# Kernel optimization log

Hardware: AMD Instinct MI355X
Metric: run time of the kernel (lower is better)

## Reference

```python
import jax, jax.numpy as jnp
import numpy as np

N, E, D, EDGE_DIM = 50000, 150000, 100, 200

def _w(key, fi, fo):
    return jax.random.normal(key, (fi, fo), dtype=jnp.float32) / np.float32(np.sqrt(fi))

def setup_inputs():
    key = jax.random.key(0)
    ks = jax.random.split(key, 40)
    inp = {}
    inp["x"] = jax.random.normal(ks[0], (N, D), dtype=jnp.float32)
    inp["msg"] = jax.random.normal(ks[1], (E, D), dtype=jnp.float32)
    # TimeEncoder: Linear(1, D)
    inp["time_w"] = _w(ks[2], 1, D)
    inp["time_b"] = jnp.zeros((D,), jnp.float32)
    # TransformerConv 1: in=100, heads=8, out=100, concat -> 800
    H1 = 8 * D
    inp["c1_qw"] = _w(ks[3], D, H1); inp["c1_qb"] = jnp.zeros((H1,), jnp.float32)
    inp["c1_kw"] = _w(ks[4], D, H1); inp["c1_kb"] = jnp.zeros((H1,), jnp.float32)
    inp["c1_vw"] = _w(ks[5], D, H1); inp["c1_vb"] = jnp.zeros((H1,), jnp.float32)
    inp["c1_ew"] = _w(ks[6], EDGE_DIM, H1)  # lin_edge has no bias in PyG
    inp["c1_sw"] = _w(ks[7], D, H1); inp["c1_sb"] = jnp.zeros((H1,), jnp.float32)
    # TransformerConv 2: in=800, heads=1, out=100, concat=False
    inp["c2_qw"] = _w(ks[8], H1, D); inp["c2_qb"] = jnp.zeros((D,), jnp.float32)
    inp["c2_kw"] = _w(ks[9], H1, D); inp["c2_kb"] = jnp.zeros((D,), jnp.float32)
    inp["c2_vw"] = _w(ks[10], H1, D); inp["c2_vb"] = jnp.zeros((D,), jnp.float32)
    inp["c2_ew"] = _w(ks[11], EDGE_DIM, D)
    inp["c2_sw"] = _w(ks[12], H1, D); inp["c2_sb"] = jnp.zeros((D,), jnp.float32)
    # LinkPredictor (in_channels=100, out=2)
    inp["lp_src_w"] = _w(ks[13], D, 2 * D); inp["lp_src_b"] = jnp.zeros((2 * D,), jnp.float32)
    inp["lp_dst_w"] = _w(ks[14], D, 2 * D); inp["lp_dst_b"] = jnp.zeros((2 * D,), jnp.float32)
    inp["lp1_w"] = _w(ks[15], 4 * D, 8 * D); inp["lp1_b"] = jnp.zeros((8 * D,), jnp.float32)
    inp["lp2_w"] = _w(ks[16], 8 * D, 2 * D); inp["lp2_b"] = jnp.zeros((2 * D,), jnp.float32)
    inp["lp3_w"] = _w(ks[17], 2 * D, D // 2); inp["lp3_b"] = jnp.zeros((D // 2,), jnp.float32)
    inp["lp4_w"] = _w(ks[18], D // 2, 2); inp["lp4_b"] = jnp.zeros((2,), jnp.float32)
    inp["last_update"] = jax.random.randint(ks[19], (N,), 0, 1000000)
    inp["t"] = jax.random.randint(ks[20], (E,), 0, 1000000)
    inp["edge_index"] = jax.random.randint(ks[21], (2, E), 0, N)
    return inp

def _tconv(x, src, dst, edge_attr, qw, qb, kw, kb, vw, vb, ew, sw, sb, heads, out_ch, concat, n):
    q = (x @ qw + qb).reshape(n, heads, out_ch)
    k = (x @ kw + kb).reshape(n, heads, out_ch)
    v = (x @ vw + vb).reshape(n, heads, out_ch)
    e = (edge_attr @ ew).reshape(-1, heads, out_ch)        # [E,H,C]
    kj = k[src] + e                                        # gather src keys + edge
    alpha = jnp.sum(q[dst] * kj, axis=-1) / np.float32(np.sqrt(out_ch))  # [E,H]
    amax = jax.ops.segment_max(alpha, dst, num_segments=n)
    ex = jnp.exp(alpha - amax[dst])
    denom = jax.ops.segment_sum(ex, dst, num_segments=n)
    a = ex / (denom[dst] + 1e-16)                          # per-dest softmax
    agg = jax.ops.segment_sum((v[src] + e) * a[..., None], dst, num_segments=n)
    out = agg.reshape(n, heads * out_ch) if concat else jnp.mean(agg, axis=1)
    return out + x @ sw + sb                               # root/skip connection

def reference(x, msg, time_w, time_b,
              c1_qw, c1_qb, c1_kw, c1_kb, c1_vw, c1_vb, c1_ew, c1_sw, c1_sb,
              c2_qw, c2_qb, c2_kw, c2_kb, c2_vw, c2_vb, c2_ew, c2_sw, c2_sb,
              lp_src_w, lp_src_b, lp_dst_w, lp_dst_b,
              lp1_w, lp1_b, lp2_w, lp2_b, lp3_w, lp3_b, lp4_w, lp4_b,
              last_update, t, edge_index):
    src, dst = edge_index[0], edge_index[1]
    rel_t = (last_update[src] - t).astype(jnp.float32)[:, None]  # [E,1]
    rel_enc = jnp.cos(rel_t @ time_w + time_b)                   # [E,D]
    edge_attr = jnp.concatenate([rel_enc, msg], axis=-1)         # [E,200]
    h = jax.nn.relu(_tconv(x, src, dst, edge_attr, c1_qw, c1_qb, c1_kw, c1_kb,
                           c1_vw, c1_vb, c1_ew, c1_sw, c1_sb, 8, D, True, N))
    h = jax.nn.relu(_tconv(h, src, dst, edge_attr, c2_qw, c2_qb, c2_kw, c2_kb,
                           c2_vw, c2_vb, c2_ew, c2_sw, c2_sb, 1, D, False, N))
    hh = jnp.concatenate([h[src] @ lp_src_w + lp_src_b,
                          h[dst] @ lp_dst_w + lp_dst_b], axis=-1)
    hh = jnp.tanh(hh @ lp1_w + lp1_b)
    hh = jnp.tanh(hh @ lp2_w + lp2_b)
    hh = jnp.tanh(hh @ lp3_w + lp3_b)
    return hh @ lp4_w + lp4_b
```

## Files before the change

### kernel.cpp

```cpp
#include <hip/hip_runtime.h>
#include <hip/hip_bf16.h>
#include <math.h>

typedef __hip_bfloat16 bf16;
typedef short s16x8 __attribute__((ext_vector_type(8)));
typedef float f32x4 __attribute__((ext_vector_type(4)));

#define NN 50000
#define EE 150000
#define EH 75000

static __device__ __forceinline__ float b2f(bf16 x){ return __bfloat162float(x); }
static __device__ __forceinline__ bf16 f2b(float x){ return __float2bfloat16(x); }
static __device__ __forceinline__ short f2s(float x){
  union { bf16 b; short s; } u; u.b = f2b(x); return u.s;
}
static __device__ __forceinline__ float u2f_lo(unsigned u){ union{unsigned i;float f;}c; c.i=u<<16; return c.f; }
static __device__ __forceinline__ float u2f_hi(unsigned u){ union{unsigned i;float f;}c; c.i=u&0xffff0000u; return c.f; }

static __device__ __forceinline__ float fast_tanh(float x){
  float a = fabsf(x);
  float e = __expf(2.0f*a);
  float t = 1.0f - __fdividef(2.0f, e + 1.0f);
  return x < 0.f ? -t : t;
}

static __device__ __forceinline__ void gload_lds16(const void* g, void* l){
  __builtin_amdgcn_global_load_lds((const __attribute__((address_space(1))) void*)g,
                                   (__attribute__((address_space(3))) void*)l, 16, 0, 0);
}

template<int N> static __device__ __forceinline__ void wait_vmcnt(){
  if constexpr(N==0) asm volatile("s_waitcnt vmcnt(0)" ::: "memory");
  else if constexpr(N==1) asm volatile("s_waitcnt vmcnt(1)" ::: "memory");
  else if constexpr(N==2) asm volatile("s_waitcnt vmcnt(2)" ::: "memory");
  else if constexpr(N==3) asm volatile("s_waitcnt vmcnt(3)" ::: "memory");
  else if constexpr(N==4) asm volatile("s_waitcnt vmcnt(4)" ::: "memory");
  else if constexpr(N==5) asm volatile("s_waitcnt vmcnt(5)" ::: "memory");
  else asm volatile("s_waitcnt vmcnt(6)" ::: "memory");
}
static __device__ __forceinline__ void wait_lgkm0(){
  asm volatile("s_waitcnt lgkmcnt(0)" ::: "memory");
}
static __device__ __forceinline__ void memfence(){
  asm volatile("" ::: "memory");
}

__global__ void k_zero(int* __restrict__ p, int n){
  int i = blockIdx.x*blockDim.x + threadIdx.x;
  if(i<n) p[i]=0;
}

__global__ void k_hist(const int* __restrict__ dst, int* __restrict__ deg){
  int i = blockIdx.x*blockDim.x + threadIdx.x;
  if(i<EE) atomicAdd(&deg[dst[i]], 1);
}

__global__ void k_scan(const int* __restrict__ deg, int* __restrict__ rowptr){
  __shared__ int part[1024];
  int tid = threadIdx.x;
  const int n = NN;
  int chunk = (n + 1023)/1024;
  int start = tid*chunk;
  int end = start + chunk; if(end > n) end = n;
  int s = 0;
  for(int i=start;i<end;i++) s += deg[i];
  part[tid] = s; __syncthreads();
  for(int off=1; off<1024; off<<=1){
    int v = (tid>=off)? part[tid-off] : 0;
    __syncthreads();
    part[tid] += v;
    __syncthreads();
  }
  int run = (tid==0)? 0 : part[tid-1];
  for(int i=start;i<end;i++){ rowptr[i]=run; run += deg[i]; }
  if(tid==0) rowptr[n] = part[1023];
}

__global__ void k_scatter(const int* __restrict__ dst, const int* __restrict__ rowptr,
                          int* __restrict__ cursor, int* __restrict__ elist){
  int e = blockIdx.x*blockDim.x + threadIdx.x;
  if(e<EE){ int d=dst[e]; int p=atomicAdd(&cursor[d],1); elist[rowptr[d]+p]=e; }
}

__global__ void k_relenc(const int* __restrict__ src, const int* __restrict__ tt,
                         const int* __restrict__ lu, const float* __restrict__ tw,
                         const float* __restrict__ tb, bf16* __restrict__ rel){
  int i = blockIdx.x*blockDim.x + threadIdx.x;
  if(i >= EE*112) return;
  int e = i/112, c = i - e*112;
  float v = 0.f;
  if(c < 100){
    float rt  = (float)(lu[src[e]] - tt[e]);
    float arg = __fadd_rn(__fmul_rn(rt, tw[c]), tb[c]);
    v = cosf(arg);
  }
  rel[i] = f2b(v);
}

__global__ void k_cvtpad(const float* __restrict__ in, int incols,
                         bf16* __restrict__ outp, int outcols, int total){
  int i = blockIdx.x*blockDim.x + threadIdx.x;
  if(i >= total) return;
  int r = i/outcols, c = i - r*outcols;
  outp[i] = f2b(c < incols ? in[(size_t)r*incols + c] : 0.f);
}

__global__ void k_wt2(const float* __restrict__ W, int K, int N, int colofs, int ncols,
                      bf16* __restrict__ WT, int kpad, int nrows){
  int i = blockIdx.x*blockDim.x + threadIdx.x;
  if(i >= nrows*kpad) return;
  int n = i / kpad, k = i - n*kpad;
  float v = (n<ncols && k<K)? W[(size_t)k*N + colofs + n] : 0.f;
  WT[i] = f2b(v);
}

__global__ void k_wtc1(const float* __restrict__ qw, const float* __restrict__ kw,
                       const float* __restrict__ vw, const float* __restrict__ sw,
                       bf16* __restrict__ outp){
  int i = blockIdx.x*blockDim.x + threadIdx.x;
  if(i >= 8*448*128) return;
  int h = i/(448*128), r = (i/128)%448, k = i&127;
  float v = 0.f;
  if(r < 400 && k < 100){
    int s = r/100, n = r - s*100;
    const float* W = s==0? qw : s==1? kw : s==2? vw : sw;
    v = W[(size_t)k*800 + h*100 + n];
  }
  outp[i] = f2b(v);
}

__global__ void k_wte(const float* __restrict__ ew, int N, int colofs,
                      bf16* __restrict__ outp){
  int i = blockIdx.x*blockDim.x + threadIdx.x;
  if(i >= 112*256) return;
  int r = i>>8, k = i&255;
  float v = 0.f;
  if(r < 100){
    if(k < 100) v = ew[(size_t)k*N + colofs + r];
    else if(k >= 128 && k < 228) v = ew[(size_t)(k-28)*N + colofs + r];
  }
  outp[i] = f2b(v);
}

__global__ void k_bstack(const float* __restrict__ b0, const float* __restrict__ b1,
                         const float* __restrict__ b2, const float* __restrict__ b3,
                         int W, int H, float* __restrict__ outp){
  int i = blockIdx.x*blockDim.x + threadIdx.x;
  if(i >= H*4*W) return;
  int h = i/(4*W), r = i - h*4*W, s = r/W, c = r - s*W;
  const float* b = s==0? b0 : s==1? b1 : s==2? b2 : b3;
  outp[i] = b[h*W + c];
}

__global__ void k_foldw(const float* __restrict__ sw, const float* __restrict__ dw,
                        const float* __restrict__ w1, bf16* __restrict__ o){
  int i = blockIdx.x*blockDim.x + threadIdx.x;
  if(i >= 800*224) return;
  int n = i/224, k = i - n*224;
  float s = 0.f;
  if(k < 100){
    for(int j=0;j<200;j++) s += sw[k*200+j]*w1[(size_t)j*800+n];
  } else if(k >= 112 && k < 212){
    int kk = k-112;
    for(int j=0;j<200;j++) s += dw[kk*200+j]*w1[(size_t)(200+j)*800+n];
  }
  o[i] = f2b(s);
}
__global__ void k_foldb(const float* __restrict__ sb, const float* __restrict__ db,
                        const float* __restrict__ w1, const float* __restrict__ b1,
                        float* __restrict__ o){
  int n = blockIdx.x*blockDim.x + threadIdx.x;
  if(n >= 800) return;
  float s = b1[n];
  for(int j=0;j<200;j++) s += sb[j]*w1[(size_t)j*800+n] + db[j]*w1[(size_t)(200+j)*800+n];
  o[n] = s;
}

template<int NT>
__global__ __launch_bounds__(256) void mm_tile(
    const bf16* __restrict__ A1, int lda1, int kv1, const int* __restrict__ g1,
    int KS,
    const bf16* __restrict__ A2b, int lda2b, int kv2b, const int* __restrict__ g2,
    const float* __restrict__ A2f, int lda2f, int kv2f,
    const bf16* __restrict__ WT, int kpad,
    const bf16* __restrict__ zbuf,
    const float* __restrict__ bias,
    bf16* __restrict__ C, int ldc,
    int M, int nvalid, int act)
{
  constexpr int BN = NT*16;
  constexpr int BPASS = (BN*4 + 255)/256;
  constexpr int ABYTES = 8192;
  constexpr int BUFSZ = ABYTES + BPASS*4096;
  __shared__ __align__(16) char lds[3*BUFSZ];

  const int tid  = threadIdx.x;
  const int wave = tid>>6, lane = tid&63;
  const int quad = lane>>4, lo = lane&15;
  const int nstrip = blockIdx.y;
  WT += (size_t)nstrip*BN*kpad;
  C  += (size_t)nstrip*BN;
  if(bias) bias += nstrip*BN;
  const int nval = nvalid - nstrip*BN;
  const int row0 = blockIdx.x*128;

  float bvr[NT];
#pragma unroll
  for(int n=0;n<NT;n++){
    int col = n*16 + lo;
    bvr[n] = (bias && col < nval) ? bias[col] : 0.f;
  }
#pragma unroll
  for(int n=0;n<NT;n++) asm volatile("" :: "v"(bvr[n]));

  const char*  a1b[2];
  const char*  a2b[2];
  const float* f2base[2];
  int acol0[2];
#pragma unroll
  for(int p=0;p<2;p++){
    int s = p*256 + tid;
    int row = s>>2, cp = s&3;
    int q = cp ^ ((row>>1)&3);
    int col0 = q*8;
    int rg = row0 + row; if(rg > M-1) rg = M-1;
    int r1 = g1 ? g1[rg] : rg;
    int r2 = g2 ? g2[rg] : rg;
    acol0[p] = col0;
    a1b[p]   = (const char*)A1 + ((size_t)r1*lda1 + col0)*2;
    a2b[p]   = A2b ? (const char*)A2b + ((size_t)r2*lda2b)*2 : nullptr;
    f2base[p]= A2f ? (A2f + (size_t)rg*lda2f) : nullptr;
  }
  const char* bbase[BPASS];
#pragma unroll
  for(int p=0;p<BPASS;p++){
    int s = p*256 + tid;
    int rb = s>>2; if(rb > BN-1) rb = BN-1;
    int cp = s&3;
    int lq = cp ^ ((rb>>1)&3);
    bbase[p] = (const char*)WT + ((size_t)rb*kpad + lq*8)*2;
  }

  f32x4 acc[2][NT];
#pragma unroll
  for(int m=0;m<2;m++)
#pragma unroll
    for(int n=0;n<NT;n++) acc[m][n] = (f32x4){0.f,0.f,0.f,0.f};

  float4 pf0[2], pf1[2];

  auto stageA1 = [&](char* buf, int kb){
#pragma unroll
    for(int p=0;p<2;p++){
      int k = kb + acol0[p];
      const char* s;
      if(k < KS) s = (k < kv1) ? (a1b[p] + (size_t)kb*2) : (const char*)zbuf;
      else { int o = k - KS; s = (o < kv2b) ? (a2b[p] + (size_t)o*2) : (const char*)zbuf; }
      gload_lds16(s, buf + p*4096 + wave*1024);
    }
  };
  auto loadA2f = [&](int kb){
#pragma unroll
    for(int p=0;p<2;p++){
      int o = kb + acol0[p] - KS;
      const float* ap = f2base[p] + o;
      pf0[p] = (o   < kv2f) ? *(const float4*)ap     : (float4){0.f,0.f,0.f,0.f};
      pf1[p] = (o+4 < kv2f) ? *(const float4*)(ap+4) : (float4){0.f,0.f,0.f,0.f};
    }
  };
  auto writeA2 = [&](char* buf){
#pragma unroll
    for(int p=0;p<2;p++){
      s16x8 v;
      v[0]=f2s(pf0[p].x); v[1]=f2s(pf0[p].y); v[2]=f2s(pf0[p].z); v[3]=f2s(pf0[p].w);
      v[4]=f2s(pf1[p].x); v[5]=f2s(pf1[p].y); v[6]=f2s(pf1[p].z); v[7]=f2s(pf1[p].w);
      *(s16x8*)(buf + p*4096 + (size_t)tid*16) = v;
    }
  };
  auto stageB = [&](char* buf, int kb){
#pragma unroll
    for(int p=0;p<BPASS;p++)
      gload_lds16(bbase[p] + (size_t)kb*2, buf + ABYTES + p*4096 + wave*1024);
  };
  auto compute = [&](const char* buf){
    s16x8 af[2];
#pragma unroll
    for(int m=0;m<2;m++){
      int rl = wave*32 + m*16 + lo;
      int cp = quad ^ ((rl>>1)&3);
      af[m] = *(const s16x8*)(buf + rl*64 + cp*16);
    }
#pragma unroll
    for(int n=0;n<NT;n++){
      int rb = n*16 + lo;
      int cp = quad ^ ((rb>>1)&3);
      s16x8 bfr = *(const s16x8*)(buf + ABYTES + rb*64 + cp*16);
      acc[0][n] = __builtin_amdgcn_mfma_f32_16x16x32_bf16(af[0], bfr, acc[0][n], 0,0,0);
      acc[1][n] = __builtin_amdgcn_mfma_f32_16x16x32_bf16(af[1], bfr, acc[1][n], 0,0,0);
    }
  };

  const int T = kpad >> 5;
  stageA1(lds, 0); stageB(lds, 0);
  if(T > 1){ stageA1(lds + BUFSZ, 32); stageB(lds + BUFSZ, 32); }

  for(int t=0; t<T; t++){
    bool nb  = (t+1 < T);
    bool nfp = nb && A2f && (((t+1)<<5) >= KS);
    if(!nb)      wait_vmcnt<0>();
    else if(nfp) wait_vmcnt<BPASS>();
    else         wait_vmcnt<2+BPASS>();
    wait_lgkm0();
    __builtin_amdgcn_s_barrier();
    memfence();
    int tp = t+2;
    bool sp  = (tp < T);
    bool spf = sp && A2f && ((tp<<5) >= KS);
    char* nb3 = lds + (tp%3)*BUFSZ;
    if(sp){
      int kb2 = tp<<5;
      if(spf) loadA2f(kb2);
      else    stageA1(nb3, kb2);
      stageB(nb3, kb2);
    }
    compute(lds + (t%3)*BUFSZ);
    if(spf) writeA2(nb3);
  }

  const int r0 = (lane&1)<<1;
#pragma unroll
  for(int n=0;n<NT;n++){
    int col  = n*16 + lo;
    int pcol = col & ~1;
    bool cok = (pcol < nval);
    float bv = bvr[n];
#pragma unroll
    for(int m=0;m<2;m++){
      float v[4];
#pragma unroll
      for(int r=0;r<4;r++){
        float t = acc[m][n][r] + bv;
        if(act==1) t = fmaxf(t, 0.f);
        else if(act==2) t = fast_tanh(t);
        v[r] = t;
      }
      unsigned mylo = (unsigned)(unsigned short)f2s(v[r0])
                    | ((unsigned)(unsigned short)f2s(v[r0+1])<<16);
      unsigned snd  = (unsigned)(unsigned short)f2s(v[r0^2])
                    | ((unsigned)(unsigned short)f2s(v[(r0^2)+1])<<16);
      unsigned got  = (unsigned)__shfl_xor((int)snd, 1);
      unsigned w0, w1;
      if(lane&1){ w0 = (got & 0xffffu) | (mylo<<16); w1 = (got>>16) | (mylo & 0xffff0000u); }
      else      { w0 = (mylo & 0xffffu) | (got<<16); w1 = (mylo>>16) | (got & 0xffff0000u); }
      if(cok){
        int prow = row0 + wave*32 + m*16 + quad*4 + r0;
        if(prow   < M) *(unsigned*)(C + (size_t)prow*ldc + pcol) = w0;
        if(prow+1 < M) *(unsigned*)(C + (size_t)(prow+1)*ldc + pcol) = w1;
      }
    }
  }
}

__global__ __launch_bounds__(256) void k_attn(
    const int* __restrict__ rowptr, const int* __restrict__ elist,
    const int* __restrict__ srcv,
    const bf16* __restrict__ qkvs, const bf16* __restrict__ eh,
    bf16* __restrict__ hout, int ldh, int colofs, int zpad)
{
  int wave = threadIdx.x>>6, lane = threadIdx.x&63;
  int node = blockIdx.x*4 + wave;
  if(node >= NN) return;
  bool act = (lane < 50);
  float q0=0.f, q1=0.f;
  const unsigned* qrow = (const unsigned*)(qkvs + (size_t)node*400);
  if(act){ unsigned u = qrow[lane]; q0=u2f_lo(u); q1=u2f_hi(u); }
  int s0 = rowptr[node], s1 = rowptr[node+1];
  float m = -3.4e38f, d = 0.f, a0 = 0.f, a1 = 0.f;
  for(int j=s0; j<s1; j++){
    int e = elist[j];
    int sn = srcv[e];
    float p = 0.f, e0=0.f, e1=0.f;
    if(act){
      unsigned uk = ((const unsigned*)(qkvs + (size_t)sn*400 + 100))[lane];
      unsigned ue = ((const unsigned*)(eh   + (size_t)e*100))[lane];
      e0=u2f_lo(ue); e1=u2f_hi(ue);
      p = q0*(u2f_lo(uk)+e0) + q1*(u2f_hi(uk)+e1);
    }
    for(int off=32; off; off>>=1) p += __shfl_xor(p, off);
    float alpha = p * 0.1f;
    float mn = fmaxf(m, alpha);
    float sc = __expf(m - mn);
    float wv = __expf(alpha - mn);
    d = d*sc + wv;
    if(act){
      unsigned uv = ((const unsigned*)(qkvs + (size_t)sn*400 + 200))[lane];
      a0 = a0*sc + wv*(u2f_lo(uv)+e0);
      a1 = a1*sc + wv*(u2f_hi(uv)+e1);
    }
    m = mn;
  }
  if(act){
    float inv = 1.f/(d + 1e-16f);
    unsigned us = ((const unsigned*)(qkvs + (size_t)node*400 + 300))[lane];
    float h0 = fmaxf(u2f_lo(us) + a0*inv, 0.f);
    float h1 = fmaxf(u2f_hi(us) + a1*inv, 0.f);
    bf16* op = hout + (size_t)node*ldh + colofs + lane*2;
    op[0] = f2b(h0); op[1] = f2b(h1);
  } else if(zpad && lane < 56){
    bf16* op = hout + (size_t)node*ldh + colofs + lane*2;
    op[0] = f2b(0.f); op[1] = f2b(0.f);
  }
}

__global__ void k_lpout(const bf16* __restrict__ t3, const float* __restrict__ w4,
                        const float* __restrict__ b4, float* __restrict__ out,
                        int base, int n){
  int i = blockIdx.x*blockDim.x + threadIdx.x;
  if(i >= n*2) return;
  int g = i>>1, j = i&1;
  const bf16* tp = t3 + (size_t)g*50;
  float s = 0.f;
  for(int k=0;k<50;k++) s += b2f(tp[k])*w4[k*2+j];
  out[(size_t)(base+g)*2 + j] = s + b4[j];
}

extern "C" void kernel_launch(void* const* d_in, const int* in_sizes, int n_in,
                              void* d_out, int out_size, void* d_ws, size_t ws_size,
                              hipStream_t stream){
  const float* x       = (const float*)d_in[0];
  const float* msg     = (const float*)d_in[1];
  const float* time_w  = (const float*)d_in[2];
  const float* time_b  = (const float*)d_in[3];
  const float* c1_qw=(const float*)d_in[4];  const float* c1_qb=(const float*)d_in[5];
  const float* c1_kw=(const float*)d_in[6];  const float* c1_kb=(const float*)d_in[7];
  const float* c1_vw=(const float*)d_in[8];  const float* c1_vb=(const float*)d_in[9];
  const float* c1_ew=(const float*)d_in[10];
  const float* c1_sw=(const float*)d_in[11]; const float* c1_sb=(const float*)d_in[12];
  const float* c2_qw=(const float*)d_in[13]; const float* c2_qb=(const float*)d_in[14];
  const float* c2_kw=(const float*)d_in[15]; const float* c2_kb=(const float*)d_in[16];
  const float* c2_vw=(const float*)d_in[17]; const float* c2_vb=(const float*)d_in[18];
  const float* c2_ew=(const float*)d_in[19];
  const float* c2_sw=(const float*)d_in[20]; const float* c2_sb=(const float*)d_in[21];
  const float* lp_src_w=(const float*)d_in[22]; const float* lp_src_b=(const float*)d_in[23];
  const float* lp_dst_w=(const float*)d_in[24]; const float* lp_dst_b=(const float*)d_in[25];
  const float* lp1_w=(const float*)d_in[26]; const float* lp1_b=(const float*)d_in[27];
  const float* lp2_w=(const float*)d_in[28]; const float* lp2_b=(const float*)d_in[29];
  const float* lp3_w=(const float*)d_in[30]; const float* lp3_b=(const float*)d_in[31];
  const float* lp4_w=(const float*)d_in[32]; const float* lp4_b=(const float*)d_in[33];
  const int* last_update=(const int*)d_in[34];
  const int* tt =(const int*)d_in[35];
  const int* edge_index=(const int*)d_in[36];
  const int* src = edge_index;
  const int* dst = edge_index + EE;
  float* out = (float*)d_out;

  char* ws = (char*)d_ws;
  bf16*  h1    = (bf16*) (ws + 0);
  bf16*  relpad= (bf16*) (ws + 80000000);
  bf16*  eh    = (bf16*) (ws + 113600000);
  bf16*  qkvs  = (bf16*) (ws + 143600000);
  bf16*  h2p   = (bf16*) (ws + 183600000);
  bf16*  xb    = (bf16*) (ws + 183600000);
  int*   rowptr= (int*)  (ws + 194800000);
  int*   elist = (int*)  (ws + 195000064);
  int*   deg   = (int*)  (ws + 195600064);
  int*   cursor= (int*)  (ws + 195800064);
  bf16* c1all  = (bf16*)(ws + 196000064);
  bf16* c1eall = (bf16*)(ws + 196917568);
  bf16* c2all  = (bf16*)(ws + 197376320);
  bf16* c2e    = (bf16*)(ws + 198179136);
  bf16* lp1tF  = (bf16*)(ws + 198351168);
  bf16* lp2t   = (bf16*)(ws + 199268672);
  bf16* lp3t   = (bf16*)(ws + 199670080);
  float* c1ball= (float*)(ws + 199702848);
  float* c2ball= (float*)(ws + 199715648);
  bf16* zbuf   = (bf16*)(ws + 199717248);
  float* lp1c  = (float*)(ws + 199717312);
  bf16* lt1 = (bf16*)(ws + 0);
  bf16* lt2 = (bf16*)(ws + 120000000);
  bf16* lt3 = (bf16*)(ws + 150000000);

  k_wtc1<<<(8*448*128+255)/256,256,0,stream>>>(c1_qw,c1_kw,c1_vw,c1_sw,c1all);
  for(int h=0; h<8; h++)
    k_wte<<<(112*256+255)/256,256,0,stream>>>(c1_ew, 800, h*100, c1eall + (size_t)h*112*256);
  k_wte<<<(112*256+255)/256,256,0,stream>>>(c2_ew, 100, 0, c2e);
  k_wt2<<<(100*800+255)/256,256,0,stream>>>(c2_qw,800,100,0,100,c2all,         800,100);
  k_wt2<<<(100*800+255)/256,256,0,stream>>>(c2_kw,800,100,0,100,c2all+100*800, 800,100);
  k_wt2<<<(100*800+255)/256,256,0,stream>>>(c2_vw,800,100,0,100,c2all+200*800, 800,100);
  k_wt2<<<(100*800+255)/256,256,0,stream>>>(c2_sw,800,100,0,100,c2all+300*800, 800,100);
  k_wt2<<<(48*800+255)/256,256,0,stream>>>(c2_sw,800,100,0,0,   c2all+400*800, 800,48);
  k_wt2<<<(224*800+255)/256,256,0,stream>>>(lp2_w,800,200,0,200,lp2t,800,224);
  k_wt2<<<(64*224+255)/256,256,0,stream>>>(lp3_w,200,50,0,50,lp3t,224,64);
  k_foldw<<<(800*224+255)/256,256,0,stream>>>(lp_src_w, lp_dst_w, lp1_w, lp1tF);
  k_foldb<<<(800+255)/256,256,0,stream>>>(lp_src_b, lp_dst_b, lp1_w, lp1_b, lp1c);
  k_bstack<<<(3200+255)/256,256,0,stream>>>(c1_qb,c1_kb,c1_vb,c1_sb,100,8,c1ball);
  k_bstack<<<(400+255)/256,256,0,stream>>>(c2_qb,c2_kb,c2_vb,c2_sb,100,1,c2ball);
  k_zero<<<1,64,0,stream>>>((int*)zbuf, 16);
  k_cvtpad<<<(NN*112+255)/256,256,0,stream>>>(x, 100, xb, 112, NN*112);

  k_zero   <<<(NN+255)/256, 256, 0, stream>>>(deg, NN);
  k_zero   <<<(NN+255)/256, 256, 0, stream>>>(cursor, NN);
  k_hist   <<<(EE+255)/256, 256, 0, stream>>>(dst, deg);
  k_scan   <<<1, 1024, 0, stream>>>(deg, rowptr);
  k_scatter<<<(EE+255)/256, 256, 0, stream>>>(dst, rowptr, cursor, elist);

  k_relenc<<<(EE*112+255)/256, 256, 0, stream>>>(src, tt, last_update, time_w, time_b, relpad);

  int gN = (NN + 127)/128;
  int gE = (EE + 127)/128;
  int gL = (EH + 127)/128;
  int gA = (NN + 3)/4;

  for(int h=0; h<8; h++){
    mm_tile<9><<<dim3(gN,3),256,0,stream>>>(xb,112,112,nullptr, 128,
        nullptr,0,0,nullptr, nullptr,0,0,
        c1all + (size_t)h*448*128, 128, zbuf, c1ball + h*400, qkvs,400, NN,400,0);
    mm_tile<7><<<dim3(gE,1),256,0,stream>>>(relpad,112,112,nullptr, 128,
        nullptr,0,0,nullptr, msg,100,100,
        c1eall + (size_t)h*112*256, 256, zbuf, nullptr, eh,100, EE,100,0);
    k_attn<<<gA,256,0,stream>>>(rowptr, elist, src, qkvs, eh, h1, 800, h*100, 0);
  }

  mm_tile<9><<<dim3(gN,3),256,0,stream>>>(h1,800,800,nullptr, 800,
      nullptr,0,0,nullptr, nullptr,0,0,
      c2all,800, zbuf, c2ball, qkvs,400, NN,400,0);
  mm_tile<7><<<dim3(gE,1),256,0,stream>>>(relpad,112,112,nullptr, 128,
      nullptr,0,0,nullptr, msg,100,100,
      c2e,256, zbuf, nullptr, eh,100, EE,100,0);
  k_attn<<<gA,256,0,stream>>>(rowptr, elist, src, qkvs, eh, h2p, 112, 0, 1);

  for(int half=0; half<2; half++){
    const int* esrc = src + half*EH;
    const int* edst = dst + half*EH;
    mm_tile<10><<<dim3(gL,5),256,0,stream>>>(h2p,112,112,esrc, 112,
        h2p,112,112,edst, nullptr,0,0,
        lp1tF,224, zbuf, lp1c, lt1,800, EH,800,2);
    mm_tile<7><<<dim3(gL,2),256,0,stream>>>(lt1,800,800,nullptr, 800,
        nullptr,0,0,nullptr, nullptr,0,0,
        lp2t,800, zbuf, lp2_b, lt2,200, EH,200,2);
    mm_tile<4><<<dim3(gL,1),256,0,stream>>>(lt2,200,200,nullptr, 224,
        nullptr,0,0,nullptr, nullptr,0,0,
        lp3t,224, zbuf, lp3_b, lt3,50, EH,50,2);
    k_lpout<<<(EH*2+255)/256,256,0,stream>>>(lt3, lp4_w, lp4_b, out, half*EH, EH);
  }

  (void)in_sizes; (void)n_in; (void)out_size; (void)ws_size;
}
```

Before: 2.025 ms.

## Sort edge features by destination and hoist skip projection out of head loop

The edge-feature GEMM now gathers rows through the destination-sorted edge list, so attention reads edge embeddings contiguously by CSR position. Source indices are stored in sorted order, which removes the elist indirection in the attention loop. The skip projection for layer 1 is computed once as a single wide GEMM written straight into h1, and layer 2 gets its own GEMM into h2p. The per-head QKV GEMM therefore shrinks from 400 to 300 columns, and attention reads the skip term back from the output buffer. In exchange the edge GEMM does gathered A loads, and an extra array and several extra launches are added.

```diff
diff --git a/kernel.cpp b/kernel.cpp
--- a/kernel.cpp
+++ b/kernel.cpp
@@ -77,10 +77,16 @@
   if(tid==0) rowptr[n] = part[1023];
 }
 
-__global__ void k_scatter(const int* __restrict__ dst, const int* __restrict__ rowptr,
-                          int* __restrict__ cursor, int* __restrict__ elist){
+__global__ void k_scatter(const int* __restrict__ dst, const int* __restrict__ srcv,
+                          const int* __restrict__ rowptr,
+                          int* __restrict__ cursor, int* __restrict__ elist,
+                          int* __restrict__ ssrc){
   int e = blockIdx.x*blockDim.x + threadIdx.x;
-  if(e<EE){ int d=dst[e]; int p=atomicAdd(&cursor[d],1); elist[rowptr[d]+p]=e; }
+  if(e<EE){
+    int d=dst[e]; int p=atomicAdd(&cursor[d],1);
+    int pos = rowptr[d]+p;
+    elist[pos]=e; ssrc[pos]=srcv[e];
+  }
 }
 
 __global__ void k_relenc(const int* __restrict__ src, const int* __restrict__ tt,
@@ -116,15 +122,14 @@
 }
 
 __global__ void k_wtc1(const float* __restrict__ qw, const float* __restrict__ kw,
-                       const float* __restrict__ vw, const float* __restrict__ sw,
-                       bf16* __restrict__ outp){
-  int i = blockIdx.x*blockDim.x + threadIdx.x;
-  if(i >= 8*448*128) return;
-  int h = i/(448*128), r = (i/128)%448, k = i&127;
+                       const float* __restrict__ vw, bf16* __restrict__ outp){
+  int i = blockIdx.x*blockDim.x + threadIdx.x;
+  if(i >= 8*320*128) return;
+  int h = i/(320*128), r = (i/128)%320, k = i&127;
   float v = 0.f;
-  if(r < 400 && k < 100){
+  if(r < 300 && k < 100){
     int s = r/100, n = r - s*100;
-    const float* W = s==0? qw : s==1? kw : s==2? vw : sw;
+    const float* W = s==0? qw : s==1? kw : vw;
     v = W[(size_t)k*800 + h*100 + n];
   }
   outp[i] = f2b(v);
@@ -143,13 +148,13 @@
   outp[i] = f2b(v);
 }
 
-__global__ void k_bstack(const float* __restrict__ b0, const float* __restrict__ b1,
-                         const float* __restrict__ b2, const float* __restrict__ b3,
-                         int W, int H, float* __restrict__ outp){
-  int i = blockIdx.x*blockDim.x + threadIdx.x;
-  if(i >= H*4*W) return;
-  int h = i/(4*W), r = i - h*4*W, s = r/W, c = r - s*W;
-  const float* b = s==0? b0 : s==1? b1 : s==2? b2 : b3;
+__global__ void k_bstack3(const float* __restrict__ b0, const float* __restrict__ b1,
+                          const float* __restrict__ b2, int W, int H,
+                          float* __restrict__ outp){
+  int i = blockIdx.x*blockDim.x + threadIdx.x;
+  if(i >= H*3*W) return;
+  int h = i/(3*W), r = i - h*3*W, s = r/W, c = r - s*W;
+  const float* b = s==0? b0 : s==1? b1 : b2;
   outp[i] = b[h*W + c];
 }
 
@@ -178,7 +183,8 @@
 }
 
 template<int NT>
-__global__ __launch_bounds__(256) void mm_tile(
+static __device__ void mm_body(
+    char* lds, int bx, int nstrip,
     const bf16* __restrict__ A1, int lda1, int kv1, const int* __restrict__ g1,
     int KS,
     const bf16* __restrict__ A2b, int lda2b, int kv2b, const int* __restrict__ g2,
@@ -193,17 +199,15 @@
   constexpr int BPASS = (BN*4 + 255)/256;
   constexpr int ABYTES = 8192;
   constexpr int BUFSZ = ABYTES + BPASS*4096;
-  __shared__ __align__(16) char lds[3*BUFSZ];
 
   const int tid  = threadIdx.x;
   const int wave = tid>>6, lane = tid&63;
   const int quad = lane>>4, lo = lane&15;
-  const int nstrip = blockIdx.y;
   WT += (size_t)nstrip*BN*kpad;
   C  += (size_t)nstrip*BN;
   if(bias) bias += nstrip*BN;
   const int nval = nvalid - nstrip*BN;
-  const int row0 = blockIdx.x*128;
+  const int row0 = bx*128;
 
   float bvr[NT];
 #pragma unroll
@@ -215,7 +219,7 @@
   for(int n=0;n<NT;n++) asm volatile("" :: "v"(bvr[n]));
 
   const char*  a1b[2];
-  const char*  a2b[2];
+  const char*  a2bp[2];
   const float* f2base[2];
   int acol0[2];
 #pragma unroll
@@ -229,8 +233,8 @@
     int r2 = g2 ? g2[rg] : rg;
     acol0[p] = col0;
     a1b[p]   = (const char*)A1 + ((size_t)r1*lda1 + col0)*2;
-    a2b[p]   = A2b ? (const char*)A2b + ((size_t)r2*lda2b)*2 : nullptr;
-    f2base[p]= A2f ? (A2f + (size_t)rg*lda2f) : nullptr;
+    a2bp[p]  = A2b ? (const char*)A2b + ((size_t)r2*lda2b)*2 : nullptr;
+    f2base[p]= A2f ? (A2f + (size_t)r2*lda2f) : nullptr;
   }
   const char* bbase[BPASS];
 #pragma unroll
@@ -256,7 +260,7 @@
       int k = kb + acol0[p];
       const char* s;
       if(k < KS) s = (k < kv1) ? (a1b[p] + (size_t)kb*2) : (const char*)zbuf;
-      else { int o = k - KS; s = (o < kv2b) ? (a2b[p] + (size_t)o*2) : (const char*)zbuf; }
+      else { int o = k - KS; s = (o < kv2b) ? (a2bp[p] + (size_t)o*2) : (const char*)zbuf; }
       gload_lds16(s, buf + p*4096 + wave*1024);
     }
   };
@@ -362,10 +366,24 @@
   }
 }
 
+template<int NT>
+__global__ __launch_bounds__(256) void mm_tile(
+    const bf16* A1, int lda1, int kv1, const int* g1, int KS,
+    const bf16* A2b, int lda2b, int kv2b, const int* g2,
+    const float* A2f, int lda2f, int kv2f,
+    const bf16* WT, int kpad, const bf16* zbuf, const float* bias,
+    bf16* C, int ldc, int M, int nvalid, int act)
+{
+  constexpr int BUFSZ = 8192 + ((NT*16*4+255)/256)*4096;
+  __shared__ __align__(16) char lds[3*BUFSZ];
+  mm_body<NT>(lds, blockIdx.x, blockIdx.y, A1,lda1,kv1,g1, KS,
+              A2b,lda2b,kv2b,g2, A2f,lda2f,kv2f, WT,kpad, zbuf, bias,
+              C,ldc, M,nvalid,act);
+}
+
 __global__ __launch_bounds__(256) void k_attn(
-    const int* __restrict__ rowptr, const int* __restrict__ elist,
-    const int* __restrict__ srcv,
-    const bf16* __restrict__ qkvs, const bf16* __restrict__ eh,
+    const int* __restrict__ rowptr, const int* __restrict__ ssrc,
+    const bf16* __restrict__ qkv, const bf16* __restrict__ ehc,
     bf16* __restrict__ hout, int ldh, int colofs, int zpad)
 {
   int wave = threadIdx.x>>6, lane = threadIdx.x&63;
@@ -373,17 +391,16 @@
   if(node >= NN) return;
   bool act = (lane < 50);
   float q0=0.f, q1=0.f;
-  const unsigned* qrow = (const unsigned*)(qkvs + (size_t)node*400);
+  const unsigned* qrow = (const unsigned*)(qkv + (size_t)node*300);
   if(act){ unsigned u = qrow[lane]; q0=u2f_lo(u); q1=u2f_hi(u); }
   int s0 = rowptr[node], s1 = rowptr[node+1];
   float m = -3.4e38f, d = 0.f, a0 = 0.f, a1 = 0.f;
   for(int j=s0; j<s1; j++){
-    int e = elist[j];
-    int sn = srcv[e];
+    int sn = ssrc[j];
     float p = 0.f, e0=0.f, e1=0.f;
     if(act){
-      unsigned uk = ((const unsigned*)(qkvs + (size_t)sn*400 + 100))[lane];
-      unsigned ue = ((const unsigned*)(eh   + (size_t)e*100))[lane];
+      unsigned uk = ((const unsigned*)(qkv + (size_t)sn*300 + 100))[lane];
+      unsigned ue = ((const unsigned*)(ehc + (size_t)j*100))[lane];
       e0=u2f_lo(ue); e1=u2f_hi(ue);
       p = q0*(u2f_lo(uk)+e0) + q1*(u2f_hi(uk)+e1);
     }
@@ -394,7 +411,7 @@
     float wv = __expf(alpha - mn);
     d = d*sc + wv;
     if(act){
-      unsigned uv = ((const unsigned*)(qkvs + (size_t)sn*400 + 200))[lane];
+      unsigned uv = ((const unsigned*)(qkv + (size_t)sn*300 + 200))[lane];
       a0 = a0*sc + wv*(u2f_lo(uv)+e0);
       a1 = a1*sc + wv*(u2f_hi(uv)+e1);
     }
@@ -402,7 +419,7 @@
   }
   if(act){
     float inv = 1.f/(d + 1e-16f);
-    unsigned us = ((const unsigned*)(qkvs + (size_t)node*400 + 300))[lane];
+    unsigned us = ((const unsigned*)(hout + (size_t)node*ldh + colofs))[lane];
     float h0 = fmaxf(u2f_lo(us) + a0*inv, 0.f);
     float h1 = fmaxf(u2f_hi(us) + a1*inv, 0.f);
     bf16* op = hout + (size_t)node*ldh + colofs + lane*2;
@@ -458,44 +475,48 @@
   char* ws = (char*)d_ws;
   bf16*  h1    = (bf16*) (ws + 0);
   bf16*  relpad= (bf16*) (ws + 80000000);
-  bf16*  eh    = (bf16*) (ws + 113600000);
-  bf16*  qkvs  = (bf16*) (ws + 143600000);
+  bf16*  ehc   = (bf16*) (ws + 113600000);
+  bf16*  qkv   = (bf16*) (ws + 143600000);
   bf16*  h2p   = (bf16*) (ws + 183600000);
   bf16*  xb    = (bf16*) (ws + 183600000);
   int*   rowptr= (int*)  (ws + 194800000);
   int*   elist = (int*)  (ws + 195000064);
-  int*   deg   = (int*)  (ws + 195600064);
-  int*   cursor= (int*)  (ws + 195800064);
-  bf16* c1all  = (bf16*)(ws + 196000064);
-  bf16* c1eall = (bf16*)(ws + 196917568);
-  bf16* c2all  = (bf16*)(ws + 197376320);
-  bf16* c2e    = (bf16*)(ws + 198179136);
-  bf16* lp1tF  = (bf16*)(ws + 198351168);
-  bf16* lp2t   = (bf16*)(ws + 199268672);
-  bf16* lp3t   = (bf16*)(ws + 199670080);
-  float* c1ball= (float*)(ws + 199702848);
-  float* c2ball= (float*)(ws + 199715648);
-  bf16* zbuf   = (bf16*)(ws + 199717248);
-  float* lp1c  = (float*)(ws + 199717312);
+  int*   ssrc  = (int*)  (ws + 195600064);
+  int*   deg   = (int*)  (ws + 196200064);
+  int*   cursor= (int*)  (ws + 196400064);
+  bf16* c1all  = (bf16*)(ws + 196600064);
+  bf16* c1eall = (bf16*)(ws + 197255424);
+  bf16* c1swt  = (bf16*)(ws + 197714176);
+  bf16* c2all  = (bf16*)(ws + 197918976);
+  bf16* c2swt  = (bf16*)(ws + 198430976);
+  bf16* c2e    = (bf16*)(ws + 198610176);
+  bf16* lp1tF  = (bf16*)(ws + 198667520);
+  bf16* lp2t   = (bf16*)(ws + 199025920);
+  bf16* lp3t   = (bf16*)(ws + 199384320);
+  float* c1ball= (float*)(ws + 199412992);
+  float* c2ball= (float*)(ws + 199422592);
+  float* lp1c  = (float*)(ws + 199423808);
+  bf16* zbuf   = (bf16*)(ws + 199427008);
   bf16* lt1 = (bf16*)(ws + 0);
   bf16* lt2 = (bf16*)(ws + 120000000);
   bf16* lt3 = (bf16*)(ws + 150000000);
 
-  k_wtc1<<<(8*448*128+255)/256,256,0,stream>>>(c1_qw,c1_kw,c1_vw,c1_sw,c1all);
+  k_wtc1<<<(8*320*128+255)/256,256,0,stream>>>(c1_qw,c1_kw,c1_vw,c1all);
   for(int h=0; h<8; h++)
     k_wte<<<(112*256+255)/256,256,0,stream>>>(c1_ew, 800, h*100, c1eall + (size_t)h*112*256);
   k_wte<<<(112*256+255)/256,256,0,stream>>>(c2_ew, 100, 0, c2e);
+  k_wt2<<<(800*128+255)/256,256,0,stream>>>(c1_sw,100,800,0,800,c1swt,128,800);
   k_wt2<<<(100*800+255)/256,256,0,stream>>>(c2_qw,800,100,0,100,c2all,         800,100);
   k_wt2<<<(100*800+255)/256,256,0,stream>>>(c2_kw,800,100,0,100,c2all+100*800, 800,100);
   k_wt2<<<(100*800+255)/256,256,0,stream>>>(c2_vw,800,100,0,100,c2all+200*800, 800,100);
-  k_wt2<<<(100*800+255)/256,256,0,stream>>>(c2_sw,800,100,0,100,c2all+300*800, 800,100);
-  k_wt2<<<(48*800+255)/256,256,0,stream>>>(c2_sw,800,100,0,0,   c2all+400*800, 800,48);
+  k_wt2<<<(20*800+255)/256,256,0,stream>>>(c2_qw,800,100,0,0,   c2all+300*800, 800,20);
+  k_wt2<<<(112*800+255)/256,256,0,stream>>>(c2_sw,800,100,0,100,c2swt,800,112);
   k_wt2<<<(224*800+255)/256,256,0,stream>>>(lp2_w,800,200,0,200,lp2t,800,224);
   k_wt2<<<(64*224+255)/256,256,0,stream>>>(lp3_w,200,50,0,50,lp3t,224,64);
   k_foldw<<<(800*224+255)/256,256,0,stream>>>(lp_src_w, lp_dst_w, lp1_w, lp1tF);
   k_foldb<<<(800+255)/256,256,0,stream>>>(lp_src_b, lp_dst_b, lp1_w, lp1_b, lp1c);
-  k_bstack<<<(3200+255)/256,256,0,stream>>>(c1_qb,c1_kb,c1_vb,c1_sb,100,8,c1ball);
-  k_bstack<<<(400+255)/256,256,0,stream>>>(c2_qb,c2_kb,c2_vb,c2_sb,100,1,c2ball);
+  k_bstack3<<<(8*300+255)/256,256,0,stream>>>(c1_qb,c1_kb,c1_vb,100,8,c1ball);
+  k_bstack3<<<(300+255)/256,256,0,stream>>>(c2_qb,c2_kb,c2_vb,100,1,c2ball);
   k_zero<<<1,64,0,stream>>>((int*)zbuf, 16);
   k_cvtpad<<<(NN*112+255)/256,256,0,stream>>>(x, 100, xb, 112, NN*112);
 
@@ -503,7 +524,7 @@
   k_zero   <<<(NN+255)/256, 256, 0, stream>>>(cursor, NN);
   k_hist   <<<(EE+255)/256, 256, 0, stream>>>(dst, deg);
   k_scan   <<<1, 1024, 0, stream>>>(deg, rowptr);
-  k_scatter<<<(EE+255)/256, 256, 0, stream>>>(dst, rowptr, cursor, elist);
+  k_scatter<<<(EE+255)/256, 256, 0, stream>>>(dst, src, rowptr, cursor, elist, ssrc);
 
   k_relenc<<<(EE*112+255)/256, 256, 0, stream>>>(src, tt, last_update, time_w, time_b, relpad);
 
@@ -512,23 +533,30 @@
   int gL = (EH + 127)/128;
   int gA = (NN + 3)/4;
 
+  mm_tile<10><<<dim3(gN,5),256,0,stream>>>(xb,112,112,nullptr, 128,
+      nullptr,0,0,nullptr, nullptr,0,0,
+      c1swt,128, zbuf, c1_sb, h1,800, NN,800,0);
+
   for(int h=0; h<8; h++){
-    mm_tile<9><<<dim3(gN,3),256,0,stream>>>(xb,112,112,nullptr, 128,
+    mm_tile<10><<<dim3(gN,2),256,0,stream>>>(xb,112,112,nullptr, 128,
         nullptr,0,0,nullptr, nullptr,0,0,
-        c1all + (size_t)h*448*128, 128, zbuf, c1ball + h*400, qkvs,400, NN,400,0);
-    mm_tile<7><<<dim3(gE,1),256,0,stream>>>(relpad,112,112,nullptr, 128,
-        nullptr,0,0,nullptr, msg,100,100,
-        c1eall + (size_t)h*112*256, 256, zbuf, nullptr, eh,100, EE,100,0);
-    k_attn<<<gA,256,0,stream>>>(rowptr, elist, src, qkvs, eh, h1, 800, h*100, 0);
-  }
-
-  mm_tile<9><<<dim3(gN,3),256,0,stream>>>(h1,800,800,nullptr, 800,
+        c1all + (size_t)h*320*128, 128, zbuf, c1ball + h*300, qkv,300, NN,300,0);
+    mm_tile<7><<<dim3(gE,1),256,0,stream>>>(relpad,112,112,elist, 128,
+        nullptr,0,0,elist, msg,100,100,
+        c1eall + (size_t)h*112*256, 256, zbuf, nullptr, ehc,100, EE,100,0);
+    k_attn<<<gA,256,0,stream>>>(rowptr, ssrc, qkv, ehc, h1, 800, h*100, 0);
+  }
+
+  mm_tile<10><<<dim3(gN,2),256,0,stream>>>(h1,800,800,nullptr, 800,
       nullptr,0,0,nullptr, nullptr,0,0,
-      c2all,800, zbuf, c2ball, qkvs,400, NN,400,0);
-  mm_tile<7><<<dim3(gE,1),256,0,stream>>>(relpad,112,112,nullptr, 128,
-      nullptr,0,0,nullptr, msg,100,100,
-      c2e,256, zbuf, nullptr, eh,100, EE,100,0);
-  k_attn<<<gA,256,0,stream>>>(rowptr, elist, src, qkvs, eh, h2p, 112, 0, 1);
+      c2all,800, zbuf, c2ball, qkv,300, NN,300,0);
+  mm_tile<7><<<dim3(gE,1),256,0,stream>>>(relpad,112,112,elist, 128,
+      nullptr,0,0,elist, msg,100,100,
+      c2e,256, zbuf, nullptr, ehc,100, EE,100,0);
+  mm_tile<7><<<dim3(gN,1),256,0,stream>>>(h1,800,800,nullptr, 800,
+      nullptr,0,0,nullptr, nullptr,0,0,
+      c2swt,800, zbuf, c2_sb, h2p,112, NN,100,0);
+  k_attn<<<gA,256,0,stream>>>(rowptr, ssrc, qkv, ehc, h2p, 112, 0, 1);
 
   for(int half=0; half<2; half++){
     const int* esrc = src + half*EH;
```

After: 2.054 ms. Within noise of the previous version (+1.4%).
